# Performance work log

Hardware: AMD Instinct MI355X
Metric: run time of the kernel (lower is better)

## Reference

```python
import jax, jax.numpy as jnp
import numpy as np

N = 100000   # total nodes across all graphs
E = 200000   # directed edges
B = 128      # number of graphs in the batch
IN1, IN2 = 128, 128
IN = IN1 + IN2      # in_feats = 256 (x || x_da)
HID = 64
OUT = 64


def setup_inputs() -> dict:
    key = jax.random.key(0)
    ks = jax.random.split(key, 6)
    x = jax.random.normal(ks[0], (N, IN1), jnp.float32)
    x_da = jax.random.normal(ks[1], (N, IN2), jnp.float32)
    edge_index = jax.random.randint(ks[2], (2, E), 0, N, dtype=jnp.int32)
    # equal, sorted, non-empty segments (graph ids) -- mirrors sorted PyG batch vector
    batch = (jnp.arange(N, dtype=jnp.int32) * B) // N
    # root node of graph b = first node of its segment
    rootindex = (jnp.arange(B, dtype=jnp.int32) * N) // B
    s1 = 1.0 / np.sqrt(IN)
    W1 = jax.random.uniform(ks[3], (IN, HID), jnp.float32, -s1, s1)
    b1 = jnp.zeros((HID,), jnp.float32)
    s2 = 1.0 / np.sqrt(HID + IN)
    W2 = jax.random.uniform(ks[4], (HID + IN, OUT), jnp.float32, -s2, s2)
    b2 = jnp.zeros((OUT,), jnp.float32)
    return dict(x=x, x_da=x_da, edge_index=edge_index, batch=batch,
                rootindex=rootindex, W1=W1, b1=b1, W2=W2, b2=b2)


def gcn_conv(x, edge_index, W, b):
    """PyG GCNConv: symmetric-normalized A+I message passing after a linear."""
    n = x.shape[0]
    h = x @ W                                   # [n, out] linear first (as in PyG)
    src, dst = edge_index[0], edge_index[1]
    # degree on target nodes, +1 for the added self loop
    deg = jnp.zeros((n,), h.dtype).at[dst].add(jnp.ones((src.shape[0],), h.dtype)) + 1.0
    dinv = jax.lax.rsqrt(deg)
    norm = dinv[src] * dinv[dst]                # [E]
    agg = jnp.zeros_like(h).at[dst].add(h[src] * norm[:, None])
    agg = agg + h * (dinv * dinv)[:, None]      # self-loop term: 1/deg
    return agg + b


def reference(x, x_da, edge_index, batch, rootindex, W1, b1, W2, b2):
    x0 = jnp.concatenate([x, x_da], axis=1)     # [N, IN]
    x1 = x0                                     # saved original features
    h = gcn_conv(x0, edge_index, W1, b1)        # [N, HID]
    x2 = h                                      # saved conv1 output
    # vectorized root-feature broadcast: replaces the python per-graph loop
    root1 = x1[rootindex[batch]]                # [N, IN]
    h = jax.nn.relu(jnp.concatenate([h, root1], axis=1))  # [N, HID+IN]
    # F.dropout with training=False is identity (eval mode)
    h = gcn_conv(h, edge_index, W2, b2)         # [N, OUT]
    h = jax.nn.relu(h)
    root2 = x2[rootindex[batch]]                # [N, HID]
    h = jnp.concatenate([h, root2], axis=1)     # [N, OUT+HID]
    # scatter_mean over graph ids
    sums = jax.ops.segment_sum(h, batch, num_segments=B)
    counts = jax.ops.segment_sum(jnp.ones((h.shape[0], 1), h.dtype), batch, num_segments=B)
    return sums / counts                        # [B, OUT+HID]
```

## Files before the change

### kernel.cpp

```cpp
#include <hip/hip_runtime.h>

#define IN1 128
#define K1 256
#define HID 64
#define MCH 16

typedef __attribute__((ext_vector_type(8))) __bf16 bf16x8;
typedef __attribute__((ext_vector_type(4))) float f32x4;

__device__ __forceinline__ int swz(int row, int k, int ldk) {
    return (row * ldk + k) ^ ((row & 7) << 3);
}

__global__ __launch_bounds__(256) void zero_counts(int* counts, int N) {
    int i = blockIdx.x * 256 + threadIdx.x;
    if (i < N) counts[i] = 0;
}

__global__ __launch_bounds__(256) void count_edges(const int* __restrict__ ei, int* counts, int E) {
    int e = blockIdx.x * 256 + threadIdx.x;
    if (e < E) atomicAdd(&counts[ei[E + e]], 1);
}

__global__ __launch_bounds__(256) void dinv_k(const int* __restrict__ counts, float* dinv, int N) {
    int i = blockIdx.x * 256 + threadIdx.x;
    if (i < N) dinv[i] = rsqrtf((float)counts[i] + 1.0f);
}

__global__ __launch_bounds__(256) void block_sums(const int* __restrict__ counts,
                                                  int* __restrict__ bsum, int N) {
    __shared__ int sh[256];
    int i = blockIdx.x * 256 + threadIdx.x;
    sh[threadIdx.x] = (i < N) ? counts[i] : 0;
    __syncthreads();
    for (int off = 128; off > 0; off >>= 1) {
        if (threadIdx.x < off) sh[threadIdx.x] += sh[threadIdx.x + off];
        __syncthreads();
    }
    if (threadIdx.x == 0) bsum[blockIdx.x] = sh[0];
}

__global__ __launch_bounds__(512) void scan_bsums(const int* __restrict__ bsum,
                                                  int* __restrict__ boff, int nb) {
    __shared__ int sh[512];
    int t = threadIdx.x;
    int v = (t < nb) ? bsum[t] : 0;
    sh[t] = v;
    __syncthreads();
    for (int off = 1; off < 512; off <<= 1) {
        int u = (t >= off) ? sh[t - off] : 0;
        __syncthreads();
        sh[t] += u;
        __syncthreads();
    }
    if (t < nb) boff[t] = sh[t] - v;
}

__global__ __launch_bounds__(256) void write_rowstart(const int* __restrict__ counts,
                                                      const int* __restrict__ boff,
                                                      int* __restrict__ rowstart, int N, int E) {
    __shared__ int sh[256];
    int i = blockIdx.x * 256 + threadIdx.x;
    int t = threadIdx.x;
    int v = (i < N) ? counts[i] : 0;
    sh[t] = v;
    __syncthreads();
    for (int off = 1; off < 256; off <<= 1) {
        int u = (t >= off) ? sh[t - off] : 0;
        __syncthreads();
        sh[t] += u;
        __syncthreads();
    }
    if (i < N) rowstart[i] = boff[blockIdx.x] + sh[t] - v;
    if (i == 0) rowstart[N] = E;
}

__global__ __launch_bounds__(256) void scatter_csr(const int* __restrict__ ei,
                                                   const int* __restrict__ rowstart,
                                                   const float* __restrict__ dinv,
                                                   int* counts,
                                                   int* __restrict__ csr_src,
                                                   float* __restrict__ csr_w, int E) {
    int e = blockIdx.x * 256 + threadIdx.x;
    if (e >= E) return;
    int s = ei[e], d = ei[E + e];
    int pos = rowstart[d] + atomicSub(&counts[d], 1) - 1;
    csr_src[pos] = s;
    csr_w[pos] = dinv[s];
}

__global__ __launch_bounds__(256) void prep_w(const float* __restrict__ W1,
                                              const float* __restrict__ W2,
                                              __bf16* __restrict__ w1img,
                                              __bf16* __restrict__ w2img) {
    int tid = blockIdx.x * 256 + threadIdx.x;
    if (tid < 64 * K1) {
        int k = tid >> 6, n = tid & 63;
        w1img[swz(n, k, K1)] = (__bf16)W1[tid];
    } else if (tid < 64 * K1 + 64 * 64) {
        int e = tid - 64 * K1;
        int k = e >> 6, n = e & 63;
        w2img[swz(n, k, 64)] = (__bf16)W2[e];
    }
}

__global__ __launch_bounds__(256) void gemm1_mfma(const float* __restrict__ x,
                                                  const float* __restrict__ xda,
                                                  const __bf16* __restrict__ w1img,
                                                  float* __restrict__ h1, int N) {
    __shared__ __bf16 Ws[64 * K1];
    int tid = threadIdx.x;
#pragma unroll
    for (int i = 0; i < 8; ++i)
        reinterpret_cast<bf16x8*>(Ws)[i * 256 + tid] =
            reinterpret_cast<const bf16x8*>(w1img)[i * 256 + tid];
    __syncthreads();

    int row0 = blockIdx.x * 64;
    int w = tid >> 6, l = tid & 63;
    int lr = l & 15, lg = l >> 4;
    int arow = row0 + w * 16 + lr;
    bool rowok = arow < N;
    const float4* a0 = reinterpret_cast<const float4*>(x + (size_t)arow * IN1);
    const float4* a1 = reinterpret_cast<const float4*>(xda + (size_t)arow * IN1);
    f32x4 acc[4] = {};
#pragma unroll
    for (int t = 0; t < 8; ++t) {
        int k0 = t * 32 + lg * 8;
        float4 fa = make_float4(0.f, 0.f, 0.f, 0.f), fb = fa;
        if (rowok) {
            const float4* src = (t < 4) ? (a0 + (k0 >> 2)) : (a1 + ((k0 - 128) >> 2));
            fa = src[0];
            fb = src[1];
        }
        bf16x8 af;
        af[0] = (__bf16)fa.x; af[1] = (__bf16)fa.y; af[2] = (__bf16)fa.z; af[3] = (__bf16)fa.w;
        af[4] = (__bf16)fb.x; af[5] = (__bf16)fb.y; af[6] = (__bf16)fb.z; af[7] = (__bf16)fb.w;
#pragma unroll
        for (int c = 0; c < 4; ++c) {
            bf16x8 bfr = *reinterpret_cast<const bf16x8*>(&Ws[swz(c * 16 + lr, k0, K1)]);
            acc[c] = __builtin_amdgcn_mfma_f32_16x16x32_bf16(af, bfr, acc[c], 0, 0, 0);
        }
    }
#pragma unroll
    for (int c = 0; c < 4; ++c) {
#pragma unroll
        for (int r = 0; r < 4; ++r) {
            int row = row0 + w * 16 + lg * 4 + r;
            if (row < N) h1[(size_t)row * HID + c * 16 + lr] = acc[c][r];
        }
    }
}

__global__ __launch_bounds__(256) void gemm2_mfma(const float* __restrict__ x2,
                                                  const __bf16* __restrict__ w2img,
                                                  const float* __restrict__ rb2,
                                                  const int* __restrict__ batch,
                                                  float* __restrict__ h2, int N) {
    __shared__ __bf16 Ws[64 * 64];
    int tid = threadIdx.x;
#pragma unroll
    for (int i = 0; i < 2; ++i)
        reinterpret_cast<bf16x8*>(Ws)[i * 256 + tid] =
            reinterpret_cast<const bf16x8*>(w2img)[i * 256 + tid];
    __syncthreads();

    int row0 = blockIdx.x * 64;
    int w = tid >> 6, l = tid & 63;
    int lr = l & 15, lg = l >> 4;
    int arow = row0 + w * 16 + lr;
    bool rowok = arow < N;
    const float4* a0 = reinterpret_cast<const float4*>(x2 + (size_t)arow * HID);
    f32x4 acc[4] = {};
#pragma unroll
    for (int t = 0; t < 2; ++t) {
        int k0 = t * 32 + lg * 8;
        float4 fa = make_float4(0.f, 0.f, 0.f, 0.f), fb = fa;
        if (rowok) {
            fa = a0[k0 >> 2];
            fb = a0[(k0 >> 2) + 1];
        }
        bf16x8 af;
        af[0] = (__bf16)fmaxf(fa.x, 0.f); af[1] = (__bf16)fmaxf(fa.y, 0.f);
        af[2] = (__bf16)fmaxf(fa.z, 0.f); af[3] = (__bf16)fmaxf(fa.w, 0.f);
        af[4] = (__bf16)fmaxf(fb.x, 0.f); af[5] = (__bf16)fmaxf(fb.y, 0.f);
        af[6] = (__bf16)fmaxf(fb.z, 0.f); af[7] = (__bf16)fmaxf(fb.w, 0.f);
#pragma unroll
        for (int c = 0; c < 4; ++c) {
            bf16x8 bfr = *reinterpret_cast<const bf16x8*>(&Ws[swz(c * 16 + lr, k0, 64)]);
            acc[c] = __builtin_amdgcn_mfma_f32_16x16x32_bf16(af, bfr, acc[c], 0, 0, 0);
        }
    }
#pragma unroll
    for (int r = 0; r < 4; ++r) {
        int row = row0 + w * 16 + lg * 4 + r;
        if (row >= N) continue;
        int b = batch[row];
        const float* rv = rb2 + (size_t)b * HID;
#pragma unroll
        for (int c = 0; c < 4; ++c)
            h2[(size_t)row * HID + c * 16 + lr] = acc[c][r] + rv[c * 16 + lr];
    }
}

__global__ __launch_bounds__(256) void gather(const int* __restrict__ rowstart,
                                              const int* __restrict__ csr_src,
                                              const float* __restrict__ csr_w,
                                              const float* __restrict__ h,
                                              const float* __restrict__ dinv,
                                              const float* __restrict__ bias,
                                              float* __restrict__ out, int N) {
    int t = blockIdx.x * 256 + threadIdx.x;
    int i = t >> 4, c = t & 15;
    if (i >= N) return;
    float di = dinv[i];
    float s2 = di * di;
    float4 v = reinterpret_cast<const float4*>(h + (size_t)i * HID)[c];
    float4 bv = reinterpret_cast<const float4*>(bias)[c];
    float4 acc = make_float4(fmaf(v.x, s2, bv.x), fmaf(v.y, s2, bv.y),
                             fmaf(v.z, s2, bv.z), fmaf(v.w, s2, bv.w));
    int k0 = rowstart[i], k1 = rowstart[i + 1];
    for (int k = k0; k < k1; ++k) {
        int s = csr_src[k];
        float w = csr_w[k] * di;
        float4 hv = reinterpret_cast<const float4*>(h + (size_t)s * HID)[c];
        acc.x = fmaf(hv.x, w, acc.x);
        acc.y = fmaf(hv.y, w, acc.y);
        acc.z = fmaf(hv.z, w, acc.z);
        acc.w = fmaf(hv.w, w, acc.w);
    }
    reinterpret_cast<float4*>(out + (size_t)i * HID)[c] = acc;
}

__global__ __launch_bounds__(64) void rb2_k(const float* __restrict__ x,
                                            const float* __restrict__ xda,
                                            const int* __restrict__ rootindex,
                                            const float* __restrict__ W2,
                                            float* __restrict__ rb2) {
    int b = blockIdx.x;
    int j = threadIdx.x;
    int root = rootindex[b];
    const float* xr = x + (size_t)root * IN1;
    const float* dr = xda + (size_t)root * IN1;
    float acc = 0.f;
    for (int k = 0; k < IN1; ++k) {
        float v = fmaxf(xr[k], 0.f);
        acc = fmaf(v, W2[(size_t)(HID + k) * HID + j], acc);
    }
    for (int k = 0; k < IN1; ++k) {
        float v = fmaxf(dr[k], 0.f);
        acc = fmaf(v, W2[(size_t)(HID + IN1 + k) * HID + j], acc);
    }
    rb2[b * HID + j] = acc;
}

__global__ __launch_bounds__(256) void seg_bounds(const int* __restrict__ batch,
                                                  int* __restrict__ segs, int N, int B) {
    int b = blockIdx.x * 256 + threadIdx.x;
    if (b > B) return;
    if (b == B) { segs[B] = N; return; }
    int lo = 0, hi = N;
    while (lo < hi) {
        int mid = (lo + hi) >> 1;
        if (batch[mid] < b) lo = mid + 1; else hi = mid;
    }
    segs[b] = lo;
}

__global__ __launch_bounds__(256) void mean_part(const float* __restrict__ agg2,
                                                 const int* __restrict__ segs,
                                                 float* __restrict__ part) {
    int b = blockIdx.x / MCH, c = blockIdx.x % MCH;
    int s = segs[b], e = segs[b + 1];
    long len = e - s;
    int cs = s + (int)(len * c / MCH);
    int ce = s + (int)(len * (c + 1) / MCH);
    int f = threadIdx.x & 63, g = threadIdx.x >> 6;
    float p = 0.f;
    for (int i = cs + g; i < ce; i += 4)
        p += fmaxf(agg2[(size_t)i * HID + f], 0.f);
    __shared__ float red[4][64];
    red[g][f] = p;
    __syncthreads();
    if (g == 0)
        part[((size_t)b * MCH + c) * 64 + f] = red[0][f] + red[1][f] + red[2][f] + red[3][f];
}

__global__ __launch_bounds__(128) void mean_fin(const float* __restrict__ part,
                                                const float* __restrict__ x2,
                                                const int* __restrict__ segs,
                                                const int* __restrict__ rootindex,
                                                float* __restrict__ out) {
    int b = blockIdx.x;
    int f = threadIdx.x;
    if (f < 64) {
        float s = 0.f;
#pragma unroll
        for (int c = 0; c < MCH; ++c) s += part[((size_t)b * MCH + c) * 64 + f];
        out[b * 128 + f] = s / (float)(segs[b + 1] - segs[b]);
    } else {
        int root = rootindex[b];
        out[b * 128 + f] = x2[(size_t)root * HID + (f - 64)];
    }
}

extern "C" void kernel_launch(void* const* d_in, const int* in_sizes, int n_in,
                              void* d_out, int out_size, void* d_ws, size_t ws_size,
                              hipStream_t stream) {
    const float* x    = (const float*)d_in[0];
    const float* xda  = (const float*)d_in[1];
    const int*   ei   = (const int*)d_in[2];
    const int*   batch= (const int*)d_in[3];
    const int*   root = (const int*)d_in[4];
    const float* W1   = (const float*)d_in[5];
    const float* b1   = (const float*)d_in[6];
    const float* W2   = (const float*)d_in[7];
    const float* b2   = (const float*)d_in[8];
    float* out = (float*)d_out;

    int N = in_sizes[3];
    int E = in_sizes[2] / 2;
    int B = in_sizes[4];

    int gN   = (N + 255) / 256;
    int gE   = (E + 255) / 256;
    int gN16 = (N * 16 + 255) / 256;
    int gM   = (N + 63) / 64;
    int nb   = gN;

    auto align = [](size_t v) { return (v + 255) & ~(size_t)255; };
    char* w = (char*)d_ws;
    float* dinv   = (float*)w;  w += align((size_t)N * 4);
    int*   counts = (int*)w;    w += align((size_t)N * 4);
    int*   rowst  = (int*)w;    w += align((size_t)(N + 1) * 4);
    int*   bsum   = (int*)w;    w += align((size_t)nb * 4);
    int*   boff   = (int*)w;    w += align((size_t)nb * 4);
    int*   csr_src= (int*)w;    w += align((size_t)E * 4);
    float* csr_w  = (float*)w;  w += align((size_t)E * 4);
    float* bufA   = (float*)w;  w += align((size_t)N * HID * 4);
    float* bufB   = (float*)w;  w += align((size_t)N * HID * 4);
    float* bufC   = (float*)w;  w += align((size_t)N * HID * 4);
    float* rb2    = (float*)w;  w += align((size_t)B * HID * 4);
    int*   segs   = (int*)w;    w += align((size_t)(B + 1) * 4);
    __bf16* w1img = (__bf16*)w; w += align((size_t)64 * K1 * 2);
    __bf16* w2img = (__bf16*)w; w += align((size_t)64 * 64 * 2);
    float* part   = (float*)w;  w += align((size_t)B * MCH * 64 * 4);

    zero_counts<<<gN, 256, 0, stream>>>(counts, N);
    count_edges<<<gE, 256, 0, stream>>>(ei, counts, E);
    dinv_k<<<gN, 256, 0, stream>>>(counts, dinv, N);
    block_sums<<<gN, 256, 0, stream>>>(counts, bsum, N);
    scan_bsums<<<1, 512, 0, stream>>>(bsum, boff, nb);
    write_rowstart<<<gN, 256, 0, stream>>>(counts, boff, rowst, N, E);
    scatter_csr<<<gE, 256, 0, stream>>>(ei, rowst, dinv, counts, csr_src, csr_w, E);
    seg_bounds<<<1, 256, 0, stream>>>(batch, segs, N, B);
    prep_w<<<(64 * K1 + 64 * 64 + 255) / 256, 256, 0, stream>>>(W1, W2, w1img, w2img);
    rb2_k<<<B, 64, 0, stream>>>(x, xda, root, W2, rb2);

    gemm1_mfma<<<gM, 256, 0, stream>>>(x, xda, w1img, bufA, N);
    gather<<<gN16, 256, 0, stream>>>(rowst, csr_src, csr_w, bufA, dinv, b1, bufB, N);

    gemm2_mfma<<<gM, 256, 0, stream>>>(bufB, w2img, rb2, batch, bufA, N);
    gather<<<gN16, 256, 0, stream>>>(rowst, csr_src, csr_w, bufA, dinv, b2, bufC, N);

    mean_part<<<B * MCH, 256, 0, stream>>>(bufC, segs, part);
    mean_fin<<<B, 128, 0, stream>>>(part, bufB, segs, root, out);
}
```

Measured before the change: 256.9 us.

## Store intermediates in bf16, enlarge GEMM tiles, and merge small setup kernels

```diff
diff --git a/kernel.cpp b/kernel.cpp
--- a/kernel.cpp
+++ b/kernel.cpp
@@ -4,17 +4,15 @@
 #define K1 256
 #define HID 64
 #define MCH 16
+#define BM1 128
 
 typedef __attribute__((ext_vector_type(8))) __bf16 bf16x8;
+typedef __attribute__((ext_vector_type(4))) __bf16 bf16x4;
+typedef __attribute__((ext_vector_type(8))) unsigned short u16x8;
 typedef __attribute__((ext_vector_type(4))) float f32x4;
 
 __device__ __forceinline__ int swz(int row, int k, int ldk) {
     return (row * ldk + k) ^ ((row & 7) << 3);
-}
-
-__global__ __launch_bounds__(256) void zero_counts(int* counts, int N) {
-    int i = blockIdx.x * 256 + threadIdx.x;
-    if (i < N) counts[i] = 0;
 }
 
 __global__ __launch_bounds__(256) void count_edges(const int* __restrict__ ei, int* counts, int E) {
@@ -22,16 +20,14 @@
     if (e < E) atomicAdd(&counts[ei[E + e]], 1);
 }
 
-__global__ __launch_bounds__(256) void dinv_k(const int* __restrict__ counts, float* dinv, int N) {
-    int i = blockIdx.x * 256 + threadIdx.x;
-    if (i < N) dinv[i] = rsqrtf((float)counts[i] + 1.0f);
-}
-
-__global__ __launch_bounds__(256) void block_sums(const int* __restrict__ counts,
-                                                  int* __restrict__ bsum, int N) {
+__global__ __launch_bounds__(256) void block_sums_dinv(const int* __restrict__ counts,
+                                                       int* __restrict__ bsum,
+                                                       float* __restrict__ dinv, int N) {
     __shared__ int sh[256];
     int i = blockIdx.x * 256 + threadIdx.x;
-    sh[threadIdx.x] = (i < N) ? counts[i] : 0;
+    int v = (i < N) ? counts[i] : 0;
+    if (i < N) dinv[i] = rsqrtf((float)v + 1.0f);
+    sh[threadIdx.x] = v;
     __syncthreads();
     for (int off = 128; off > 0; off >>= 1) {
         if (threadIdx.x < off) sh[threadIdx.x] += sh[threadIdx.x + off];
@@ -40,20 +36,34 @@
     if (threadIdx.x == 0) bsum[blockIdx.x] = sh[0];
 }
 
-__global__ __launch_bounds__(512) void scan_bsums(const int* __restrict__ bsum,
-                                                  int* __restrict__ boff, int nb) {
-    __shared__ int sh[512];
-    int t = threadIdx.x;
-    int v = (t < nb) ? bsum[t] : 0;
-    sh[t] = v;
-    __syncthreads();
-    for (int off = 1; off < 512; off <<= 1) {
-        int u = (t >= off) ? sh[t - off] : 0;
+__global__ __launch_bounds__(512) void scan_and_segs(const int* __restrict__ bsum,
+                                                     int* __restrict__ boff, int nb,
+                                                     const int* __restrict__ batch,
+                                                     int* __restrict__ segs, int N, int B) {
+    if (blockIdx.x == 0) {
+        __shared__ int sh[512];
+        int t = threadIdx.x;
+        int v = (t < nb) ? bsum[t] : 0;
+        sh[t] = v;
         __syncthreads();
-        sh[t] += u;
-        __syncthreads();
-    }
-    if (t < nb) boff[t] = sh[t] - v;
+        for (int off = 1; off < 512; off <<= 1) {
+            int u = (t >= off) ? sh[t - off] : 0;
+            __syncthreads();
+            sh[t] += u;
+            __syncthreads();
+        }
+        if (t < nb) boff[t] = sh[t] - v;
+    } else {
+        int b = threadIdx.x;
+        if (b > B) return;
+        if (b == B) { segs[B] = N; return; }
+        int lo = 0, hi = N;
+        while (lo < hi) {
+            int mid = (lo + hi) >> 1;
+            if (batch[mid] < b) lo = mid + 1; else hi = mid;
+        }
+        segs[b] = lo;
+    }
 }
 
 __global__ __launch_bounds__(256) void write_rowstart(const int* __restrict__ counts,
@@ -107,7 +117,7 @@
 __global__ __launch_bounds__(256) void gemm1_mfma(const float* __restrict__ x,
                                                   const float* __restrict__ xda,
                                                   const __bf16* __restrict__ w1img,
-                                                  float* __restrict__ h1, int N) {
+                                                  __bf16* __restrict__ h1, int N) {
     __shared__ __bf16 Ws[64 * K1];
     int tid = threadIdx.x;
 #pragma unroll
@@ -116,47 +126,64 @@
             reinterpret_cast<const bf16x8*>(w1img)[i * 256 + tid];
     __syncthreads();
 
-    int row0 = blockIdx.x * 64;
     int w = tid >> 6, l = tid & 63;
     int lr = l & 15, lg = l >> 4;
-    int arow = row0 + w * 16 + lr;
-    bool rowok = arow < N;
-    const float4* a0 = reinterpret_cast<const float4*>(x + (size_t)arow * IN1);
-    const float4* a1 = reinterpret_cast<const float4*>(xda + (size_t)arow * IN1);
-    f32x4 acc[4] = {};
-#pragma unroll
-    for (int t = 0; t < 8; ++t) {
-        int k0 = t * 32 + lg * 8;
-        float4 fa = make_float4(0.f, 0.f, 0.f, 0.f), fb = fa;
-        if (rowok) {
-            const float4* src = (t < 4) ? (a0 + (k0 >> 2)) : (a1 + ((k0 - 128) >> 2));
-            fa = src[0];
-            fb = src[1];
-        }
-        bf16x8 af;
-        af[0] = (__bf16)fa.x; af[1] = (__bf16)fa.y; af[2] = (__bf16)fa.z; af[3] = (__bf16)fa.w;
-        af[4] = (__bf16)fb.x; af[5] = (__bf16)fb.y; af[6] = (__bf16)fb.z; af[7] = (__bf16)fb.w;
-#pragma unroll
-        for (int c = 0; c < 4; ++c) {
-            bf16x8 bfr = *reinterpret_cast<const bf16x8*>(&Ws[swz(c * 16 + lr, k0, K1)]);
-            acc[c] = __builtin_amdgcn_mfma_f32_16x16x32_bf16(af, bfr, acc[c], 0, 0, 0);
-        }
-    }
-#pragma unroll
-    for (int c = 0; c < 4; ++c) {
-#pragma unroll
-        for (int r = 0; r < 4; ++r) {
-            int row = row0 + w * 16 + lg * 4 + r;
-            if (row < N) h1[(size_t)row * HID + c * 16 + lr] = acc[c][r];
-        }
-    }
-}
-
-__global__ __launch_bounds__(256) void gemm2_mfma(const float* __restrict__ x2,
+    int rbase = blockIdx.x * BM1 + w * 32;
+    const float4 z4 = make_float4(0.f, 0.f, 0.f, 0.f);
+    f32x4 acc[2][4] = {};
+    float4 ax[2][8];
+
+#pragma unroll
+    for (int half = 0; half < 2; ++half) {
+        const float* base = half ? xda : x;
+#pragma unroll
+        for (int g = 0; g < 2; ++g) {
+            int arow = rbase + g * 16 + lr;
+            bool ok = arow < N;
+            const float4* p = reinterpret_cast<const float4*>(base + (size_t)arow * IN1);
+#pragma unroll
+            for (int t = 0; t < 4; ++t) {
+                ax[g][2 * t]     = ok ? p[t * 8 + lg * 2]     : z4;
+                ax[g][2 * t + 1] = ok ? p[t * 8 + lg * 2 + 1] : z4;
+            }
+        }
+#pragma unroll
+        for (int t = 0; t < 4; ++t) {
+            int k0 = half * 128 + t * 32 + lg * 8;
+            bf16x8 bfr[4];
+#pragma unroll
+            for (int c = 0; c < 4; ++c)
+                bfr[c] = *reinterpret_cast<const bf16x8*>(&Ws[swz(c * 16 + lr, k0, K1)]);
+#pragma unroll
+            for (int g = 0; g < 2; ++g) {
+                float4 fa = ax[g][2 * t], fb = ax[g][2 * t + 1];
+                bf16x8 af;
+                af[0] = (__bf16)fa.x; af[1] = (__bf16)fa.y;
+                af[2] = (__bf16)fa.z; af[3] = (__bf16)fa.w;
+                af[4] = (__bf16)fb.x; af[5] = (__bf16)fb.y;
+                af[6] = (__bf16)fb.z; af[7] = (__bf16)fb.w;
+#pragma unroll
+                for (int c = 0; c < 4; ++c)
+                    acc[g][c] = __builtin_amdgcn_mfma_f32_16x16x32_bf16(af, bfr[c], acc[g][c], 0, 0, 0);
+            }
+        }
+    }
+#pragma unroll
+    for (int g = 0; g < 2; ++g)
+#pragma unroll
+        for (int c = 0; c < 4; ++c)
+#pragma unroll
+            for (int r = 0; r < 4; ++r) {
+                int row = rbase + g * 16 + lg * 4 + r;
+                if (row < N) h1[(size_t)row * HID + c * 16 + lr] = (__bf16)acc[g][c][r];
+            }
+}
+
+__global__ __launch_bounds__(256) void gemm2_mfma(const __bf16* __restrict__ x2,
                                                   const __bf16* __restrict__ w2img,
                                                   const float* __restrict__ rb2,
                                                   const int* __restrict__ batch,
-                                                  float* __restrict__ h2, int N) {
+                                                  __bf16* __restrict__ h2, int N) {
     __shared__ __bf16 Ws[64 * 64];
     int tid = threadIdx.x;
 #pragma unroll
@@ -165,71 +192,78 @@
             reinterpret_cast<const bf16x8*>(w2img)[i * 256 + tid];
     __syncthreads();
 
-    int row0 = blockIdx.x * 64;
     int w = tid >> 6, l = tid & 63;
     int lr = l & 15, lg = l >> 4;
-    int arow = row0 + w * 16 + lr;
-    bool rowok = arow < N;
-    const float4* a0 = reinterpret_cast<const float4*>(x2 + (size_t)arow * HID);
-    f32x4 acc[4] = {};
+    int rbase = blockIdx.x * BM1 + w * 32;
+    f32x4 acc[2][4] = {};
 #pragma unroll
     for (int t = 0; t < 2; ++t) {
         int k0 = t * 32 + lg * 8;
-        float4 fa = make_float4(0.f, 0.f, 0.f, 0.f), fb = fa;
-        if (rowok) {
-            fa = a0[k0 >> 2];
-            fb = a0[(k0 >> 2) + 1];
-        }
-        bf16x8 af;
-        af[0] = (__bf16)fmaxf(fa.x, 0.f); af[1] = (__bf16)fmaxf(fa.y, 0.f);
-        af[2] = (__bf16)fmaxf(fa.z, 0.f); af[3] = (__bf16)fmaxf(fa.w, 0.f);
-        af[4] = (__bf16)fmaxf(fb.x, 0.f); af[5] = (__bf16)fmaxf(fb.y, 0.f);
-        af[6] = (__bf16)fmaxf(fb.z, 0.f); af[7] = (__bf16)fmaxf(fb.w, 0.f);
-#pragma unroll
-        for (int c = 0; c < 4; ++c) {
-            bf16x8 bfr = *reinterpret_cast<const bf16x8*>(&Ws[swz(c * 16 + lr, k0, 64)]);
-            acc[c] = __builtin_amdgcn_mfma_f32_16x16x32_bf16(af, bfr, acc[c], 0, 0, 0);
-        }
-    }
-#pragma unroll
-    for (int r = 0; r < 4; ++r) {
-        int row = row0 + w * 16 + lg * 4 + r;
-        if (row >= N) continue;
-        int b = batch[row];
-        const float* rv = rb2 + (size_t)b * HID;
+        bf16x8 bfr[4];
 #pragma unroll
         for (int c = 0; c < 4; ++c)
-            h2[(size_t)row * HID + c * 16 + lr] = acc[c][r] + rv[c * 16 + lr];
-    }
+            bfr[c] = *reinterpret_cast<const bf16x8*>(&Ws[swz(c * 16 + lr, k0, 64)]);
+#pragma unroll
+        for (int g = 0; g < 2; ++g) {
+            int arow = rbase + g * 16 + lr;
+            u16x8 rel = {};
+            if (arow < N) {
+                u16x8 raw = *reinterpret_cast<const u16x8*>(x2 + (size_t)arow * HID + k0);
+#pragma unroll
+                for (int i = 0; i < 8; ++i)
+                    rel[i] = (raw[i] & 0x8000) ? (unsigned short)0 : raw[i];
+            }
+            bf16x8 af = *reinterpret_cast<bf16x8*>(&rel);
+#pragma unroll
+            for (int c = 0; c < 4; ++c)
+                acc[g][c] = __builtin_amdgcn_mfma_f32_16x16x32_bf16(af, bfr[c], acc[g][c], 0, 0, 0);
+        }
+    }
+#pragma unroll
+    for (int g = 0; g < 2; ++g)
+#pragma unroll
+        for (int r = 0; r < 4; ++r) {
+            int row = rbase + g * 16 + lg * 4 + r;
+            if (row >= N) continue;
+            int b = batch[row];
+            const float* rv = rb2 + (size_t)b * HID;
+#pragma unroll
+            for (int c = 0; c < 4; ++c)
+                h2[(size_t)row * HID + c * 16 + lr] = (__bf16)(acc[g][c][r] + rv[c * 16 + lr]);
+        }
 }
 
 __global__ __launch_bounds__(256) void gather(const int* __restrict__ rowstart,
                                               const int* __restrict__ csr_src,
                                               const float* __restrict__ csr_w,
-                                              const float* __restrict__ h,
+                                              const __bf16* __restrict__ h,
                                               const float* __restrict__ dinv,
                                               const float* __restrict__ bias,
-                                              float* __restrict__ out, int N) {
+                                              __bf16* __restrict__ out, int N) {
     int t = blockIdx.x * 256 + threadIdx.x;
     int i = t >> 4, c = t & 15;
     if (i >= N) return;
     float di = dinv[i];
     float s2 = di * di;
-    float4 v = reinterpret_cast<const float4*>(h + (size_t)i * HID)[c];
+    bf16x4 hv = *reinterpret_cast<const bf16x4*>(h + (size_t)i * HID + c * 4);
     float4 bv = reinterpret_cast<const float4*>(bias)[c];
-    float4 acc = make_float4(fmaf(v.x, s2, bv.x), fmaf(v.y, s2, bv.y),
-                             fmaf(v.z, s2, bv.z), fmaf(v.w, s2, bv.w));
+    float a0 = fmaf((float)hv[0], s2, bv.x);
+    float a1 = fmaf((float)hv[1], s2, bv.y);
+    float a2 = fmaf((float)hv[2], s2, bv.z);
+    float a3 = fmaf((float)hv[3], s2, bv.w);
     int k0 = rowstart[i], k1 = rowstart[i + 1];
     for (int k = k0; k < k1; ++k) {
         int s = csr_src[k];
-        float w = csr_w[k] * di;
-        float4 hv = reinterpret_cast<const float4*>(h + (size_t)s * HID)[c];
-        acc.x = fmaf(hv.x, w, acc.x);
-        acc.y = fmaf(hv.y, w, acc.y);
-        acc.z = fmaf(hv.z, w, acc.z);
-        acc.w = fmaf(hv.w, w, acc.w);
-    }
-    reinterpret_cast<float4*>(out + (size_t)i * HID)[c] = acc;
+        float wgt = csr_w[k] * di;
+        bf16x4 sv = *reinterpret_cast<const bf16x4*>(h + (size_t)s * HID + c * 4);
+        a0 = fmaf((float)sv[0], wgt, a0);
+        a1 = fmaf((float)sv[1], wgt, a1);
+        a2 = fmaf((float)sv[2], wgt, a2);
+        a3 = fmaf((float)sv[3], wgt, a3);
+    }
+    bf16x4 o;
+    o[0] = (__bf16)a0; o[1] = (__bf16)a1; o[2] = (__bf16)a2; o[3] = (__bf16)a3;
+    *reinterpret_cast<bf16x4*>(out + (size_t)i * HID + c * 4) = o;
 }
 
 __global__ __launch_bounds__(64) void rb2_k(const float* __restrict__ x,
@@ -254,20 +288,7 @@
     rb2[b * HID + j] = acc;
 }
 
-__global__ __launch_bounds__(256) void seg_bounds(const int* __restrict__ batch,
-                                                  int* __restrict__ segs, int N, int B) {
-    int b = blockIdx.x * 256 + threadIdx.x;
-    if (b > B) return;
-    if (b == B) { segs[B] = N; return; }
-    int lo = 0, hi = N;
-    while (lo < hi) {
-        int mid = (lo + hi) >> 1;
-        if (batch[mid] < b) lo = mid + 1; else hi = mid;
-    }
-    segs[b] = lo;
-}
-
-__global__ __launch_bounds__(256) void mean_part(const float* __restrict__ agg2,
+__global__ __launch_bounds__(256) void mean_part(const __bf16* __restrict__ agg2,
                                                  const int* __restrict__ segs,
                                                  float* __restrict__ part) {
     int b = blockIdx.x / MCH, c = blockIdx.x % MCH;
@@ -278,7 +299,7 @@
     int f = threadIdx.x & 63, g = threadIdx.x >> 6;
     float p = 0.f;
     for (int i = cs + g; i < ce; i += 4)
-        p += fmaxf(agg2[(size_t)i * HID + f], 0.f);
+        p += fmaxf((float)agg2[(size_t)i * HID + f], 0.f);
     __shared__ float red[4][64];
     red[g][f] = p;
     __syncthreads();
@@ -287,7 +308,7 @@
 }
 
 __global__ __launch_bounds__(128) void mean_fin(const float* __restrict__ part,
-                                                const float* __restrict__ x2,
+                                                const __bf16* __restrict__ x2,
                                                 const int* __restrict__ segs,
                                                 const int* __restrict__ rootindex,
                                                 float* __restrict__ out) {
@@ -300,7 +321,7 @@
         out[b * 128 + f] = s / (float)(segs[b + 1] - segs[b]);
     } else {
         int root = rootindex[b];
-        out[b * 128 + f] = x2[(size_t)root * HID + (f - 64)];
+        out[b * 128 + f] = (float)x2[(size_t)root * HID + (f - 64)];
     }
 }
 
@@ -325,7 +346,7 @@
     int gN   = (N + 255) / 256;
     int gE   = (E + 255) / 256;
     int gN16 = (N * 16 + 255) / 256;
-    int gM   = (N + 63) / 64;
+    int gM   = (N + BM1 - 1) / BM1;
     int nb   = gN;
 
     auto align = [](size_t v) { return (v + 255) & ~(size_t)255; };
@@ -337,23 +358,21 @@
     int*   boff   = (int*)w;    w += align((size_t)nb * 4);
     int*   csr_src= (int*)w;    w += align((size_t)E * 4);
     float* csr_w  = (float*)w;  w += align((size_t)E * 4);
-    float* bufA   = (float*)w;  w += align((size_t)N * HID * 4);
-    float* bufB   = (float*)w;  w += align((size_t)N * HID * 4);
-    float* bufC   = (float*)w;  w += align((size_t)N * HID * 4);
+    __bf16* bufA  = (__bf16*)w; w += align((size_t)N * HID * 2);
+    __bf16* bufB  = (__bf16*)w; w += align((size_t)N * HID * 2);
+    __bf16* bufC  = (__bf16*)w; w += align((size_t)N * HID * 2);
     float* rb2    = (float*)w;  w += align((size_t)B * HID * 4);
     int*   segs   = (int*)w;    w += align((size_t)(B + 1) * 4);
     __bf16* w1img = (__bf16*)w; w += align((size_t)64 * K1 * 2);
     __bf16* w2img = (__bf16*)w; w += align((size_t)64 * 64 * 2);
     float* part   = (float*)w;  w += align((size_t)B * MCH * 64 * 4);
 
-    zero_counts<<<gN, 256, 0, stream>>>(counts, N);
+    hipMemsetAsync(counts, 0, (size_t)N * 4, stream);
     count_edges<<<gE, 256, 0, stream>>>(ei, counts, E);
-    dinv_k<<<gN, 256, 0, stream>>>(counts, dinv, N);
-    block_sums<<<gN, 256, 0, stream>>>(counts, bsum, N);
-    scan_bsums<<<1, 512, 0, stream>>>(bsum, boff, nb);
+    block_sums_dinv<<<gN, 256, 0, stream>>>(counts, bsum, dinv, N);
+    scan_and_segs<<<2, 512, 0, stream>>>(bsum, boff, nb, batch, segs, N, B);
     write_rowstart<<<gN, 256, 0, stream>>>(counts, boff, rowst, N, E);
     scatter_csr<<<gE, 256, 0, stream>>>(ei, rowst, dinv, counts, csr_src, csr_w, E);
-    seg_bounds<<<1, 256, 0, stream>>>(batch, segs, N, B);
     prep_w<<<(64 * K1 + 64 * 64 + 255) / 256, 256, 0, stream>>>(W1, W2, w1img, w2img);
     rb2_k<<<B, 64, 0, stream>>>(x, xda, root, W2, rb2);
 
```

Measured after the change: 291.1 us. 13.3% more time.
